# Performance work log

Measured on AMD Instinct MI355X. Metric: run time of the kernel, lower is better.

The kernel has to match this reference:

```python
import jax, jax.numpy as jnp
import numpy as np

V, E, H, B, S = 50000, 256, 256, 64, 2048


def setup_inputs() -> dict:
    key = jax.random.key(0)
    ks = jax.random.split(key, 13)
    u = lambda k, shape: jax.random.uniform(k, shape, jnp.float32) - 0.5
    return {
        "inp": jax.random.randint(ks[0], (B,), 0, V, dtype=jnp.int64),
        "hidden": jax.random.normal(ks[1], (1, B, H), jnp.float32),
        "encoder_outputs": jax.random.normal(ks[2], (B, S, H), jnp.float32),
        "emb": jax.random.normal(ks[3], (V, E), jnp.float32),          # nn.Embedding weight
        "U": u(ks[4], (H, H)),
        "W": u(ks[5], (H, H)),
        "v": u(ks[6], (H, 1)),
        "W_ih": u(ks[7], (H, E)),   # RNN weight_ih_l0
        "W_hh": u(ks[8], (H, H)),   # RNN weight_hh_l0
        "b_ih": u(ks[9], (H,)),
        "b_hh": u(ks[10], (H,)),
        "W_out": u(ks[11], (V, H)),  # output Linear weight
        "b_out": u(ks[12], (V,)),
    }


def reference(inp, hidden, encoder_outputs, emb, U, W, v,
              W_ih, W_hh, b_ih, b_hh, W_out, b_out):
    # embedding lookup: (B, E)
    x = emb[inp]
    word_embs = x[:, None, :]                         # (B, 1, E)
    # Bahdanau additive attention (get_context)
    summed = jnp.tanh(word_embs @ U + encoder_outputs @ W)   # (B, S, H)
    e_ij = summed @ v                                        # (B, S, 1)
    alpha = jax.nn.softmax(e_ij, axis=1)                     # (B, S, 1)
    context = jnp.sum(alpha * encoder_outputs, axis=1)       # (B, H)
    # single tanh-RNN step; NOTE: original code feeds context as initial hidden,
    # ignoring the `hidden` argument when attention is enabled.
    h_new = jnp.tanh(x @ W_ih.T + b_ih + context @ W_hh.T + b_hh)  # (B, H)
    logits = h_new @ W_out.T + b_out                               # (B, V)
    return logits, h_new[None]                                     # hidden: (1, B, H)
```

## Files before the change

### kernel.cpp

```cpp
#include <hip/hip_runtime.h>
#include <hip/hip_bf16.h>
#include <math.h>

#define V_ 50000
#define E_ 256
#define H_ 256
#define B_ 64
#define S_ 2048
#define NCHK 32

typedef __attribute__((ext_vector_type(4))) float f32x4;
typedef __attribute__((ext_vector_type(16))) float f32x16;
typedef __attribute__((ext_vector_type(8))) __bf16 bf16x8;

static __device__ __forceinline__ f32x4 mfma16(bf16x8 a, bf16x8 b, f32x4 c) {
  return __builtin_amdgcn_mfma_f32_16x16x32_bf16(a, b, c, 0, 0, 0);
}
static __device__ __forceinline__ f32x16 mfma32(bf16x8 a, bf16x8 b, f32x16 c) {
  return __builtin_amdgcn_mfma_f32_32x32x16_bf16(a, b, c, 0, 0, 0);
}
static __device__ __forceinline__ float fast_tanh(float x) {
  const float e2 = __expf(2.0f * x);
  return 1.0f - 2.0f / (e2 + 1.0f);
}
static __device__ __forceinline__ void gll16(const float* g, void* l) {
  __builtin_amdgcn_global_load_lds(
      (const __attribute__((address_space(1))) void*)g,
      (__attribute__((address_space(3))) void*)l, 16, 0, 0);
}

__global__ __launch_bounds__(256) void prep_k(
    const int* __restrict__ inp, const float* __restrict__ emb,
    const float* __restrict__ U, const float* __restrict__ W_ih,
    const float* __restrict__ b_ih, const float* __restrict__ b_hh,
    float* __restrict__ xU, float* __restrict__ xWih) {
  const int b = blockIdx.x, h = threadIdx.x;
  __shared__ float xs[H_];
  xs[h] = emb[(size_t)inp[b] * E_ + h];
  __syncthreads();
  float au = 0.f, aw = 0.f;
  const float* __restrict__ wir = W_ih + (size_t)h * E_;
  for (int k = 0; k < H_; k += 4) {
    const float4 x4 = *reinterpret_cast<const float4*>(&xs[k]);
    const float4 w4 = *reinterpret_cast<const float4*>(wir + k);
    aw = fmaf(x4.x, w4.x, aw); aw = fmaf(x4.y, w4.y, aw);
    aw = fmaf(x4.z, w4.z, aw); aw = fmaf(x4.w, w4.w, aw);
    au = fmaf(x4.x, U[(size_t)(k + 0) * H_ + h], au);
    au = fmaf(x4.y, U[(size_t)(k + 1) * H_ + h], au);
    au = fmaf(x4.z, U[(size_t)(k + 2) * H_ + h], au);
    au = fmaf(x4.w, U[(size_t)(k + 3) * H_ + h], au);
  }
  xU[b * H_ + h] = au;
  xWih[b * H_ + h] = aw + b_ih[h] + b_hh[h];
}

__global__ __launch_bounds__(256) void prep_w(
    const float* __restrict__ W, __bf16* __restrict__ wt2) {
  const int idx = blockIdx.x * 256 + threadIdx.x;
  const int k = idx >> 8, col = idx & 255;
  wt2[((size_t)(k >> 3) * 256 + col) * 8 + (k & 7)] = (__bf16)W[(size_t)k * H_ + col];
}

__global__ __launch_bounds__(256, 3) void attn_fused(
    const float* __restrict__ enc, const __bf16* __restrict__ wt2,
    const float* __restrict__ xU, const float* __restrict__ vv,
    float* __restrict__ ctxp, float* __restrict__ mlout) {
  const int t = threadIdx.x;
  const int w = t >> 6, l = t & 63, l31 = l & 31, h5 = l >> 5;
  const int rg = w >> 1, cg = w & 1;

  __shared__ __align__(16) char Aring[16 * 4096];
  __shared__ float ered[2][64];
  __shared__ float wgt[64];
  __shared__ float mlS[2];

  const int ridx = blockIdx.x;
  const int b = blockIdx.y;
  const int s0 = ridx * 64;

  const int srow = t >> 2;
  const int pch = t & 3;
  const int kch = pch ^ ((srow >> 1) & 3);
  const float* __restrict__ encSrc = enc + ((size_t)b * S_ + s0 + srow) * H_ + kch * 4;

#define STAGE(ks_)                                                 \
  gll16(encSrc + (ks_) * 16, Aring + (ks_) * 4096 + w * 1024);     \
  __builtin_amdgcn_sched_barrier(0);

  STAGE(0); STAGE(1); STAGE(2); STAGE(3); STAGE(4); STAGE(5);
  bf16x8 bh[2][2][4];
#pragma unroll
  for (int hh = 0; hh < 2; ++hh)
#pragma unroll
    for (int cf = 0; cf < 4; ++cf) {
      const int col = cg * 128 + cf * 32 + l31;
      bh[0][hh][cf] = *reinterpret_cast<const bf16x8*>(
          wt2 + ((size_t)(hh * 2 + h5) * 256 + col) * 8);
    }
  __builtin_amdgcn_sched_barrier(0);

  f32x16 acc[4];
#pragma unroll
  for (int cf = 0; cf < 4; ++cf) acc[cf] = (f32x16)(0.f);

  const int r = rg * 32 + l31;
  const int sxor = (r >> 1) & 3;
  const char* arow = Aring + r * 64;

#pragma unroll
  for (int it = 0; it < 8; ++it) {
    if (it == 0)      asm volatile("s_waitcnt vmcnt(12)" ::: "memory");
    else if (it == 1) asm volatile("s_waitcnt vmcnt(20)" ::: "memory");
    else if (it <= 5) asm volatile("s_waitcnt vmcnt(28)" ::: "memory");
    else if (it == 6) asm volatile("s_waitcnt vmcnt(26)" ::: "memory");
    else              asm volatile("s_waitcnt vmcnt(24)" ::: "memory");
    __builtin_amdgcn_s_barrier();
    __builtin_amdgcn_sched_barrier(0);
    if (it <= 4) { STAGE(2 * it + 6); STAGE(2 * it + 7); }
    const int pb = it & 1;
    if (it < 7) {
#pragma unroll
      for (int hh = 0; hh < 2; ++hh) {
        const int koct = (2 * (it + 1) + hh) * 2 + h5;
#pragma unroll
        for (int cf = 0; cf < 4; ++cf) {
          const int col = cg * 128 + cf * 32 + l31;
          bh[pb ^ 1][hh][cf] = *reinterpret_cast<const bf16x8*>(
              wt2 + ((size_t)koct * 256 + col) * 8);
        }
      }
    }
    __builtin_amdgcn_sched_barrier(0);
#pragma unroll
    for (int hh = 0; hh < 2; ++hh) {
      const int ks = 2 * it + hh;
      const char* sb = arow + ks * 4096;
      const f32x4 c0 = *reinterpret_cast<const f32x4*>(sb + (((2 * h5 + 0) ^ sxor) << 4));
      const f32x4 c1 = *reinterpret_cast<const f32x4*>(sb + (((2 * h5 + 1) ^ sxor) << 4));
      bf16x8 ab;
      {
        const float xa[8] = {c0[0], c0[1], c0[2], c0[3], c1[0], c1[1], c1[2], c1[3]};
#pragma unroll
        for (int j = 0; j < 8; ++j) ab[j] = (__bf16)xa[j];
      }
#pragma unroll
      for (int cf = 0; cf < 4; ++cf) acc[cf] = mfma32(ab, bh[pb][hh][cf], acc[cf]);
    }
  }
#undef STAGE

  float xu[4], vw[4];
#pragma unroll
  for (int cf = 0; cf < 4; ++cf) {
    const int col = cg * 128 + cf * 32 + l31;
    xu[cf] = xU[b * H_ + col];
    vw[cf] = vv[col];
  }
  float rs[16];
#pragma unroll
  for (int reg = 0; reg < 16; ++reg) {
    float s = 0.f;
#pragma unroll
    for (int cf = 0; cf < 4; ++cf)
      s += fast_tanh(xu[cf] + acc[cf][reg]) * vw[cf];
    rs[reg] = s;
  }
#pragma unroll
  for (int o = 1; o < 32; o <<= 1)
#pragma unroll
    for (int reg = 0; reg < 16; ++reg)
      rs[reg] += __shfl_xor(rs[reg], o);
  if (l31 == 0) {
#pragma unroll
    for (int reg = 0; reg < 16; ++reg)
      ered[cg][rg * 32 + (reg & 3) + 8 * (reg >> 2) + 4 * h5] = rs[reg];
  }
  __syncthreads();

  if (t < 64) {
    const float es = ered[0][t] + ered[1][t];
    float m = es;
#pragma unroll
    for (int o = 1; o < 64; o <<= 1) m = fmaxf(m, __shfl_xor(m, o));
    const float we = __expf(es - m);
    float ls = we;
#pragma unroll
    for (int o = 1; o < 64; o <<= 1) ls += __shfl_xor(ls, o);
    wgt[t] = we;
    if (t == 0) { mlS[0] = m; mlS[1] = ls; }
  }
  __syncthreads();

  {
    const int h = t;
    const int ks2 = h >> 4, c2 = (h >> 2) & 3, e2 = h & 3;
    const char* base = Aring + ks2 * 4096 + e2 * 4;
    float a = 0.f;
#pragma unroll 8
    for (int s = 0; s < 64; ++s) {
      const int pch2 = c2 ^ ((s >> 1) & 3);
      const float ev = *reinterpret_cast<const float*>(
          base + (s >> 4) * 1024 + (s & 15) * 64 + pch2 * 16);
      a = fmaf(wgt[s], ev, a);
    }
    ctxp[((size_t)ridx * B_ + b) * H_ + h] = a;
  }
  if (t < 2) mlout[(ridx * B_ + b) * 2 + t] = mlS[t];
}

__global__ __launch_bounds__(256) void combine_hnew(
    const float* __restrict__ ctxp, const float* __restrict__ mlout,
    const float* __restrict__ xWih, const float* __restrict__ W_hh,
    float* __restrict__ out_h, __bf16* __restrict__ hn) {
  const int b = blockIdx.x, h = threadIdx.x;
  __shared__ float cs[H_];
  float M = -3.4e38f;
#pragma unroll
  for (int cc = 0; cc < NCHK; ++cc) M = fmaxf(M, mlout[(cc * B_ + b) * 2]);
  float num = 0.f, den = 0.f;
#pragma unroll
  for (int cc = 0; cc < NCHK; ++cc) {
    const float mw = __expf(mlout[(cc * B_ + b) * 2] - M);
    den = fmaf(mw, mlout[(cc * B_ + b) * 2 + 1], den);
    num = fmaf(mw, ctxp[((size_t)cc * B_ + b) * H_ + h], num);
  }
  cs[h] = num / den;
  __syncthreads();
  const float* __restrict__ wr = W_hh + (size_t)h * H_;
  float a = xWih[b * H_ + h];
  for (int k = 0; k < H_; k += 4) {
    const float4 w4 = *reinterpret_cast<const float4*>(wr + k);
    const float4 c4 = *reinterpret_cast<const float4*>(&cs[k]);
    a = fmaf(c4.x, w4.x, a); a = fmaf(c4.y, w4.y, a);
    a = fmaf(c4.z, w4.z, a); a = fmaf(c4.w, w4.w, a);
  }
  const float hv = fast_tanh(a);
  out_h[b * H_ + h] = hv;
  hn[b * H_ + h] = (__bf16)hv;
}

__global__ __launch_bounds__(256) void logits_mfma(
    const float* __restrict__ Wout, const float* __restrict__ bout,
    const __bf16* __restrict__ hn, float* __restrict__ logits) {
  const int v0 = blockIdx.x * 64;
  const int t = threadIdx.x;
  const int wv = t >> 6, l = t & 63, l15 = l & 15, lg = l >> 4;

  __shared__ __bf16 Wsub[8][64][32];

  {
    const int srow = t >> 2, sg = t & 3;
    const int wslot = (sg + (srow >> 1)) & 3;
    const int vc = (v0 + srow) < V_ ? (v0 + srow) : (V_ - 1);
    const float* __restrict__ wr = Wout + (size_t)vc * H_ + sg * 8;
#pragma unroll
    for (int ks = 0; ks < 8; ++ks) {
      const float4 f0 = *reinterpret_cast<const float4*>(wr + ks * 32);
      const float4 f1 = *reinterpret_cast<const float4*>(wr + ks * 32 + 4);
      const float xv[8] = {f0.x, f0.y, f0.z, f0.w, f1.x, f1.y, f1.z, f1.w};
      bf16x8 h8;
#pragma unroll
      for (int j = 0; j < 8; ++j) h8[j] = (__bf16)xv[j];
      *reinterpret_cast<bf16x8*>(&Wsub[ks][srow][wslot * 8]) = h8;
    }
  }
  __syncthreads();

  f32x4 acc[4];
#pragma unroll
  for (int i = 0; i < 4; ++i) acc[i] = (f32x4)(0.f);
  const int colb = wv * 16 + l15;
#pragma unroll
  for (int k = 0; k < 8; ++k) {
    const bf16x8 bfrag = *reinterpret_cast<const bf16x8*>(hn + (size_t)colb * H_ + k * 32 + lg * 8);
    bf16x8 ah[4];
#pragma unroll
    for (int rf = 0; rf < 4; ++rf) {
      const int rr = rf * 16 + l15;
      const int slot = (lg + (rr >> 1)) & 3;
      ah[rf] = *reinterpret_cast<const bf16x8*>(&Wsub[k][rr][slot * 8]);
    }
#pragma unroll
    for (int rf = 0; rf < 4; ++rf)
      acc[rf] = mfma16(ah[rf], bfrag, acc[rf]);
  }
#pragma unroll
  for (int rf = 0; rf < 4; ++rf) {
    const int v = v0 + rf * 16 + lg * 4;
    if (v < V_) {
      const float4 bo = *reinterpret_cast<const float4*>(bout + v);
      float4 o;
      o.x = acc[rf][0] + bo.x; o.y = acc[rf][1] + bo.y;
      o.z = acc[rf][2] + bo.z; o.w = acc[rf][3] + bo.w;
      *reinterpret_cast<float4*>(logits + (size_t)colb * V_ + v) = o;
    }
  }
}

extern "C" void kernel_launch(void* const* d_in, const int* in_sizes, int n_in,
                              void* d_out, int out_size, void* d_ws, size_t ws_size,
                              hipStream_t stream) {
  const int*   inp  = (const int*)  d_in[0];
  const float* enc  = (const float*)d_in[2];
  const float* emb  = (const float*)d_in[3];
  const float* U    = (const float*)d_in[4];
  const float* W    = (const float*)d_in[5];
  const float* v    = (const float*)d_in[6];
  const float* W_ih = (const float*)d_in[7];
  const float* W_hh = (const float*)d_in[8];
  const float* b_ih = (const float*)d_in[9];
  const float* b_hh = (const float*)d_in[10];
  const float* Wout = (const float*)d_in[11];
  const float* bout = (const float*)d_in[12];

  float* logits = (float*)d_out;
  float* out_h  = logits + (size_t)B_ * V_;

  float* ws    = (float*)d_ws;
  __bf16* wt2  = (__bf16*)ws;
  float* xU    = ws + 32768;
  float* xWih  = xU + B_ * H_;
  float* ctxp  = xWih + B_ * H_;
  float* mlout = ctxp + (size_t)NCHK * B_ * H_;
  __bf16* hn   = (__bf16*)(mlout + NCHK * B_ * 2);

  prep_k<<<dim3(B_), dim3(256), 0, stream>>>(inp, emb, U, W_ih, b_ih, b_hh, xU, xWih);
  prep_w<<<dim3(H_ * H_ / 256), dim3(256), 0, stream>>>(W, wt2);
  attn_fused<<<dim3(NCHK, B_), dim3(256), 0, stream>>>(enc, wt2, xU, v, ctxp, mlout);
  combine_hnew<<<dim3(B_), dim3(256), 0, stream>>>(ctxp, mlout, xWih, W_hh, out_h, hn);
  logits_mfma<<<dim3((V_ + 63) / 64), dim3(256), 0, stream>>>(Wout, bout, hn, logits);
}
```

Before: 98.19 us.

## Retile attention MFMA so each wave owns 64 columns across all 64 rows

Changes the warp-to-output mapping in the fused attention GEMM from a 2x2 grid (32 rows x 128 cols per wave) to a 1x4 split (64 rows x 64 cols per wave). Each wave now loads half as many W fragments per k-step but reads both A row-fragments from LDS, and the energy reduction sums four partials instead of two. The vmcnt wait thresholds are lowered to match the fewer outstanding B-fragment global loads. This cuts global/L2 traffic for the weight tiles at the cost of more LDS reads and more shuffle reductions.

```diff
diff --git a/kernel.cpp b/kernel.cpp
--- a/kernel.cpp
+++ b/kernel.cpp
@@ -67,10 +67,9 @@
     float* __restrict__ ctxp, float* __restrict__ mlout) {
   const int t = threadIdx.x;
   const int w = t >> 6, l = t & 63, l31 = l & 31, h5 = l >> 5;
-  const int rg = w >> 1, cg = w & 1;
 
   __shared__ __align__(16) char Aring[16 * 4096];
-  __shared__ float ered[2][64];
+  __shared__ float ered[4][64];
   __shared__ float wgt[64];
   __shared__ float mlS[2];
 
@@ -88,32 +87,33 @@
   __builtin_amdgcn_sched_barrier(0);
 
   STAGE(0); STAGE(1); STAGE(2); STAGE(3); STAGE(4); STAGE(5);
-  bf16x8 bh[2][2][4];
+  bf16x8 bh[2][2][2];
 #pragma unroll
   for (int hh = 0; hh < 2; ++hh)
 #pragma unroll
-    for (int cf = 0; cf < 4; ++cf) {
-      const int col = cg * 128 + cf * 32 + l31;
+    for (int cf = 0; cf < 2; ++cf) {
+      const int col = w * 64 + cf * 32 + l31;
+      const int koct = hh * 2 + h5;
       bh[0][hh][cf] = *reinterpret_cast<const bf16x8*>(
-          wt2 + ((size_t)(hh * 2 + h5) * 256 + col) * 8);
+          wt2 + ((size_t)koct * 256 + col) * 8);
     }
   __builtin_amdgcn_sched_barrier(0);
 
-  f32x16 acc[4];
-#pragma unroll
-  for (int cf = 0; cf < 4; ++cf) acc[cf] = (f32x16)(0.f);
-
-  const int r = rg * 32 + l31;
-  const int sxor = (r >> 1) & 3;
-  const char* arow = Aring + r * 64;
+  f32x16 acc[2][2];
+#pragma unroll
+  for (int rf = 0; rf < 2; ++rf)
+#pragma unroll
+    for (int cf = 0; cf < 2; ++cf) acc[rf][cf] = (f32x16)(0.f);
+
+  const int sxor = (l31 >> 1) & 3;
 
 #pragma unroll
   for (int it = 0; it < 8; ++it) {
-    if (it == 0)      asm volatile("s_waitcnt vmcnt(12)" ::: "memory");
-    else if (it == 1) asm volatile("s_waitcnt vmcnt(20)" ::: "memory");
-    else if (it <= 5) asm volatile("s_waitcnt vmcnt(28)" ::: "memory");
-    else if (it == 6) asm volatile("s_waitcnt vmcnt(26)" ::: "memory");
-    else              asm volatile("s_waitcnt vmcnt(24)" ::: "memory");
+    if (it == 0)      asm volatile("s_waitcnt vmcnt(8)" ::: "memory");
+    else if (it == 1) asm volatile("s_waitcnt vmcnt(12)" ::: "memory");
+    else if (it <= 5) asm volatile("s_waitcnt vmcnt(16)" ::: "memory");
+    else if (it == 6) asm volatile("s_waitcnt vmcnt(14)" ::: "memory");
+    else              asm volatile("s_waitcnt vmcnt(12)" ::: "memory");
     __builtin_amdgcn_s_barrier();
     __builtin_amdgcn_sched_barrier(0);
     if (it <= 4) { STAGE(2 * it + 6); STAGE(2 * it + 7); }
@@ -123,8 +123,8 @@
       for (int hh = 0; hh < 2; ++hh) {
         const int koct = (2 * (it + 1) + hh) * 2 + h5;
 #pragma unroll
-        for (int cf = 0; cf < 4; ++cf) {
-          const int col = cg * 128 + cf * 32 + l31;
+        for (int cf = 0; cf < 2; ++cf) {
+          const int col = w * 64 + cf * 32 + l31;
           bh[pb ^ 1][hh][cf] = *reinterpret_cast<const bf16x8*>(
               wt2 + ((size_t)koct * 256 + col) * 8);
         }
@@ -134,51 +134,61 @@
 #pragma unroll
     for (int hh = 0; hh < 2; ++hh) {
       const int ks = 2 * it + hh;
-      const char* sb = arow + ks * 4096;
-      const f32x4 c0 = *reinterpret_cast<const f32x4*>(sb + (((2 * h5 + 0) ^ sxor) << 4));
-      const f32x4 c1 = *reinterpret_cast<const f32x4*>(sb + (((2 * h5 + 1) ^ sxor) << 4));
-      bf16x8 ab;
-      {
+      bf16x8 ab[2];
+#pragma unroll
+      for (int rf = 0; rf < 2; ++rf) {
+        const char* sb = Aring + ks * 4096 + (rf * 32 + l31) * 64;
+        const f32x4 c0 = *reinterpret_cast<const f32x4*>(sb + (((2 * h5 + 0) ^ sxor) << 4));
+        const f32x4 c1 = *reinterpret_cast<const f32x4*>(sb + (((2 * h5 + 1) ^ sxor) << 4));
         const float xa[8] = {c0[0], c0[1], c0[2], c0[3], c1[0], c1[1], c1[2], c1[3]};
 #pragma unroll
-        for (int j = 0; j < 8; ++j) ab[j] = (__bf16)xa[j];
+        for (int j = 0; j < 8; ++j) ab[rf][j] = (__bf16)xa[j];
       }
 #pragma unroll
-      for (int cf = 0; cf < 4; ++cf) acc[cf] = mfma32(ab, bh[pb][hh][cf], acc[cf]);
+      for (int rf = 0; rf < 2; ++rf)
+#pragma unroll
+        for (int cf = 0; cf < 2; ++cf)
+          acc[rf][cf] = mfma32(ab[rf], bh[pb][hh][cf], acc[rf][cf]);
     }
   }
 #undef STAGE
 
-  float xu[4], vw[4];
-#pragma unroll
-  for (int cf = 0; cf < 4; ++cf) {
-    const int col = cg * 128 + cf * 32 + l31;
+  float xu[2], vw[2];
+#pragma unroll
+  for (int cf = 0; cf < 2; ++cf) {
+    const int col = w * 64 + cf * 32 + l31;
     xu[cf] = xU[b * H_ + col];
     vw[cf] = vv[col];
   }
-  float rs[16];
-#pragma unroll
-  for (int reg = 0; reg < 16; ++reg) {
-    float s = 0.f;
-#pragma unroll
-    for (int cf = 0; cf < 4; ++cf)
-      s += fast_tanh(xu[cf] + acc[cf][reg]) * vw[cf];
-    rs[reg] = s;
-  }
+  float rs[2][16];
+#pragma unroll
+  for (int rf = 0; rf < 2; ++rf)
+#pragma unroll
+    for (int reg = 0; reg < 16; ++reg) {
+      float s = 0.f;
+#pragma unroll
+      for (int cf = 0; cf < 2; ++cf)
+        s += fast_tanh(xu[cf] + acc[rf][cf][reg]) * vw[cf];
+      rs[rf][reg] = s;
+    }
 #pragma unroll
   for (int o = 1; o < 32; o <<= 1)
 #pragma unroll
-    for (int reg = 0; reg < 16; ++reg)
-      rs[reg] += __shfl_xor(rs[reg], o);
+    for (int rf = 0; rf < 2; ++rf)
+#pragma unroll
+      for (int reg = 0; reg < 16; ++reg)
+        rs[rf][reg] += __shfl_xor(rs[rf][reg], o);
   if (l31 == 0) {
 #pragma unroll
-    for (int reg = 0; reg < 16; ++reg)
-      ered[cg][rg * 32 + (reg & 3) + 8 * (reg >> 2) + 4 * h5] = rs[reg];
+    for (int rf = 0; rf < 2; ++rf)
+#pragma unroll
+      for (int reg = 0; reg < 16; ++reg)
+        ered[w][rf * 32 + (reg & 3) + 8 * (reg >> 2) + 4 * h5] = rs[rf][reg];
   }
   __syncthreads();
 
   if (t < 64) {
-    const float es = ered[0][t] + ered[1][t];
+    const float es = ered[0][t] + ered[1][t] + ered[2][t] + ered[3][t];
     float m = es;
 #pragma unroll
     for (int o = 1; o < 64; o <<= 1) m = fmaxf(m, __shfl_xor(m, o));
```

Result: no change. 99.64 us (+1.5%).
